# Kernel optimization log

Measured on AMD Instinct MI355X. Metric: run time of the kernel, lower is better.

The kernel has to match this reference:

```python
import jax, jax.numpy as jnp
import numpy as np

N_NODES = 100000
N_EDGES = 1600000
D_IN = 128
D_OUT = 128
EPS = 1e-5


def setup_inputs() -> dict:
    key = jax.random.key(0)
    k1, k2, k3, k4, k5 = jax.random.split(key, 5)
    x = jax.random.normal(k1, (N_NODES, D_IN), dtype=jnp.float32)
    row = jax.random.randint(k2, (N_EDGES,), 0, N_NODES, dtype=jnp.int64)
    col = jax.random.randint(k3, (N_EDGES,), 0, N_NODES, dtype=jnp.int64)
    adj_vals = jax.random.uniform(k4, (N_EDGES,), dtype=jnp.float32)
    # Xavier-uniform init for weight, zeros for bias (as in the torch module)
    limit = float(np.sqrt(6.0 / (D_IN + D_OUT)))
    weight = jax.random.uniform(k5, (D_IN, D_OUT), minval=-limit, maxval=limit, dtype=jnp.float32)
    bias = jnp.zeros((D_OUT,), dtype=jnp.float32)
    return {"x": x, "row": row, "col": col, "adj_vals": adj_vals, "weight": weight, "bias": bias}


def reference(x, row, col, adj_vals, weight, bias):
    # degree = row-sum of sparse adj
    degree = jax.ops.segment_sum(adj_vals, row, num_segments=N_NODES)
    degree = jnp.where(degree == 0, EPS, degree)
    d_inv_sqrt = (degree + EPS) ** -0.5  # [N]
    # edge-wise symmetric normalization: D^-1/2 A D^-1/2
    edge_w = d_inv_sqrt[row] * adj_vals * d_inv_sqrt[col]  # [E]
    # SpMM: gather neighbor features, scale, scatter-add to destination rows
    msgs = edge_w[:, None] * x[col]  # [E, D_IN]
    agg = jax.ops.segment_sum(msgs, row, num_segments=N_NODES)  # [N, D_IN]
    return agg @ weight + bias
```

## Files before the change

kernel.cpp:

```cpp
#include <hip/hip_runtime.h>

#define NN 100000
#define NE 1600000
#define D  128
#define EPS 1e-5f

#define NBKT   782
#define NEB    391
#define EPB_H  4096
#define NSCAN  (NBKT*NEB)
#define GRID2  299
#define CAP    2560

#define OFF_HCNT 0x0000000ULL
#define OFF_PART 0x0140000ULL
#define OFF_DINV 0x0150000ULL
#define OFF_GREC 0x0200000ULL
#define OFF_YB   0x0F00000ULL

typedef short short8 __attribute__((ext_vector_type(8)));
typedef float f32x4 __attribute__((ext_vector_type(4)));

static __device__ __forceinline__ unsigned f2bf(float f) {
    unsigned u = __float_as_uint(f);
    return (u + 0x7fffu + ((u >> 16) & 1u)) >> 16;
}

__global__ void k0h(const int* __restrict__ row, unsigned* __restrict__ hcnt) {
    __shared__ unsigned h[NBKT];
    int t = threadIdx.x, b = blockIdx.x;
    for (int i = t; i < NBKT; i += 256) h[i] = 0;
    __syncthreads();
    int ebeg = b * EPB_H;
    for (int i = t; i < EPB_H; i += 256) {
        int e = ebeg + i;
        if (e < NE) atomicAdd(&h[((unsigned)row[e]) >> 7], 1u);
    }
    __syncthreads();
    for (int i = t; i < NBKT; i += 256) hcnt[i * NEB + b] = h[i];
}

__global__ void k2a(const unsigned* __restrict__ hcnt, unsigned* __restrict__ part) {
    __shared__ unsigned s[256];
    int t = threadIdx.x;
    int gi = blockIdx.x * 1024 + t * 4;
    unsigned v = 0;
    #pragma unroll
    for (int j = 0; j < 4; ++j) if (gi + j < NSCAN) v += hcnt[gi + j];
    s[t] = v;
    __syncthreads();
    for (int d = 128; d > 0; d >>= 1) {
        if (t < d) s[t] += s[t + d];
        __syncthreads();
    }
    if (t == 0) part[blockIdx.x] = s[0];
}

__global__ void k2c(unsigned* __restrict__ hcnt, const unsigned* __restrict__ part) {
    __shared__ unsigned s[256];
    __shared__ unsigned bbase;
    int t = threadIdx.x, g = blockIdx.x;

    unsigned v = 0;
    for (int i = t; i < g; i += 256) v += part[i];
    s[t] = v;
    __syncthreads();
    for (int d = 128; d > 0; d >>= 1) {
        if (t < d) s[t] += s[t + d];
        __syncthreads();
    }
    if (t == 0) bbase = s[0];
    __syncthreads();
    unsigned base = bbase;
    __syncthreads();

    int gi = g * 1024 + t * 4;
    unsigned w[4], tot = 0;
    #pragma unroll
    for (int j = 0; j < 4; ++j) {
        w[j] = (gi + j < NSCAN) ? hcnt[gi + j] : 0;
        tot += w[j];
    }
    s[t] = tot;
    __syncthreads();
    for (int d = 1; d < 256; d <<= 1) {
        unsigned u = (t >= d) ? s[t - d] : 0;
        __syncthreads();
        s[t] += u;
        __syncthreads();
    }
    unsigned run = base + s[t] - tot;
    #pragma unroll
    for (int j = 0; j < 4; ++j) {
        if (gi + j < NSCAN) { hcnt[gi + j] = run; run += w[j]; }
    }
}

__launch_bounds__(256)
__global__ void k3(const int* __restrict__ row, const int* __restrict__ col,
                   const float* __restrict__ adj, const unsigned* __restrict__ hcnt,
                   unsigned long long* __restrict__ grec) {
    __shared__ unsigned cur[NBKT];
    int t = threadIdx.x, b = blockIdx.x;
    for (int i = t; i < NBKT; i += 256) cur[i] = hcnt[i * NEB + b];
    __syncthreads();
    int ebeg = b * EPB_H;
    for (int i = t; i < EPB_H; i += 256) {
        int e = ebeg + i;
        if (e >= NE) continue;
        unsigned r = (unsigned)row[e];
        unsigned aq = (unsigned)rintf(adj[e] * 32767.0f);
        unsigned lo = (unsigned)col[e] | (aq << 17);
        unsigned dst = atomicAdd(&cur[r >> 7], 1u);
        grec[dst] = (unsigned long long)lo | ((unsigned long long)(r & 127u) << 32);
    }
}

__launch_bounds__(256, 2)
__global__ void k1g(const float* __restrict__ x, const float* __restrict__ w,
                    const unsigned* __restrict__ hcnt,
                    const unsigned long long* __restrict__ grec,
                    float* __restrict__ dinv_g, unsigned short* __restrict__ yb) {
    __shared__ unsigned short sx[128 * 128];
    __shared__ unsigned short sw[128 * 128];
    __shared__ unsigned sdeg[128];
    __shared__ float sdv[128];
    int tid = threadIdx.x;
    int b = blockIdx.x;
    int base = b * 128;

    if (tid < 128) sdeg[tid] = 0;
    __syncthreads();
    unsigned beg = hcnt[b * NEB];
    unsigned end = (b == NBKT - 1) ? NE : hcnt[(b + 1) * NEB];
    for (unsigned p = beg + tid; p < end; p += 256) {
        unsigned long long rec = grec[p];
        atomicAdd(&sdeg[(unsigned)(rec >> 32) & 127u], ((unsigned)rec >> 17) & 0x7FFFu);
    }
    __syncthreads();
    if (tid < 128) {
        float d = (float)sdeg[tid] * (1.0f / 32767.0f);
        d = (d == 0.0f) ? EPS : d;
        float dv = rsqrtf(d + EPS);
        sdv[tid] = dv;
        int r = base + tid;
        if (r < NN) dinv_g[r] = dv;
    }

    #pragma unroll
    for (int i = 0; i < 8; ++i) {
        int task = i * 256 + tid;
        int n = task & 127, ko = task >> 7;
        const float* wp = w + (size_t)(ko * 8) * D + n;
        uint4 pk;
        pk.x = f2bf(wp[0])     | (f2bf(wp[D])     << 16);
        pk.y = f2bf(wp[2 * D]) | (f2bf(wp[3 * D]) << 16);
        pk.z = f2bf(wp[4 * D]) | (f2bf(wp[5 * D]) << 16);
        pk.w = f2bf(wp[6 * D]) | (f2bf(wp[7 * D]) << 16);
        int idx = (n * 128 + ko * 8) ^ ((n & 7) << 3);
        *(uint4*)(&sw[idx]) = pk;
    }
    #pragma unroll
    for (int i = 0; i < 8; ++i) {
        int task = i * 256 + tid;
        int ko = task & 15, r = task >> 4;
        int gr = base + r;
        float4 f0 = make_float4(0.f, 0.f, 0.f, 0.f), f1 = f0;
        if (gr < NN) {
            const float* xp = x + (size_t)gr * D + ko * 8;
            f0 = *(const float4*)xp;
            f1 = *(const float4*)(xp + 4);
        }
        uint4 pk;
        pk.x = f2bf(f0.x) | (f2bf(f0.y) << 16);
        pk.y = f2bf(f0.z) | (f2bf(f0.w) << 16);
        pk.z = f2bf(f1.x) | (f2bf(f1.y) << 16);
        pk.w = f2bf(f1.z) | (f2bf(f1.w) << 16);
        int idx = (r * 128 + ko * 8) ^ ((r & 7) << 3);
        *(uint4*)(&sx[idx]) = pk;
    }
    __syncthreads();

    int wv = tid >> 6, l = tid & 63;
    int lr = l & 15, g = l >> 4;

    f32x4 acc[2][8];
    #pragma unroll
    for (int ti = 0; ti < 2; ++ti)
        #pragma unroll
        for (int tj = 0; tj < 8; ++tj)
            acc[ti][tj] = (f32x4){0.f, 0.f, 0.f, 0.f};

    #pragma unroll
    for (int kc = 0; kc < 4; ++kc) {
        int kb = kc * 32 + g * 8;
        short8 a[2], bb[8];
        #pragma unroll
        for (int ti = 0; ti < 2; ++ti) {
            int r0 = wv * 32 + ti * 16 + lr;
            a[ti] = *(const short8*)(&sx[(r0 * 128 + kb) ^ ((r0 & 7) << 3)]);
        }
        #pragma unroll
        for (int tj = 0; tj < 8; ++tj) {
            int n0 = tj * 16 + lr;
            bb[tj] = *(const short8*)(&sw[(n0 * 128 + kb) ^ ((n0 & 7) << 3)]);
        }
        #pragma unroll
        for (int ti = 0; ti < 2; ++ti)
            #pragma unroll
            for (int tj = 0; tj < 8; ++tj)
                acc[ti][tj] = __builtin_amdgcn_mfma_f32_16x16x32_bf16(
                    a[ti], bb[tj], acc[ti][tj], 0, 0, 0);
    }

    #pragma unroll
    for (int ti = 0; ti < 2; ++ti) {
        #pragma unroll
        for (int reg = 0; reg < 4; ++reg) {
            int lrow = wv * 32 + ti * 16 + g * 4 + reg;
            int gr = base + lrow;
            if (gr < NN) {
                float dv = sdv[lrow];
                #pragma unroll
                for (int tj = 0; tj < 8; ++tj)
                    yb[(size_t)gr * D + tj * 16 + lr] =
                        (unsigned short)f2bf(acc[ti][tj][reg] * dv);
            }
        }
    }
}

__launch_bounds__(256, 4)
__global__ void k4b(const unsigned* __restrict__ hcnt, const unsigned long long* __restrict__ grec,
                    const float* __restrict__ dinv, const unsigned short* __restrict__ yb,
                    const float* __restrict__ bias, float* __restrict__ out) {
    __shared__ unsigned ecol[CAP + 16];
    __shared__ unsigned cnt[128], rb[128], cur[128], sc[128];
    int t = threadIdx.x, b = blockIdx.x;

    if (t < 128) cnt[t] = 0;
    __syncthreads();
    unsigned beg = hcnt[b * NEB];
    unsigned end = (b == NBKT - 1) ? NE : hcnt[(b + 1) * NEB];
    for (unsigned p = beg + t; p < end; p += 256)
        atomicAdd(&cnt[(unsigned)(grec[p] >> 32) & 127u], 1u);
    __syncthreads();

    if (t < 128) sc[t] = cnt[t];
    __syncthreads();
    for (int d = 1; d < 128; d <<= 1) {
        unsigned u = (t >= d && t < 128) ? sc[t - d] : 0;
        __syncthreads();
        if (t < 128) sc[t] += u;
        __syncthreads();
    }
    if (t < 128) { rb[t] = sc[t] - cnt[t]; cur[t] = sc[t] - cnt[t]; }
    __syncthreads();

    for (unsigned p = beg + t; p < end; p += 256) {
        unsigned long long rec = grec[p];
        unsigned rank = atomicAdd(&cur[(unsigned)(rec >> 32) & 127u], 1u);
        if (rank < CAP) ecol[rank] = (unsigned)rec;
    }
    __syncthreads();

    int grp = t >> 4, lq = t & 15;
    for (int k = 0; k < 8; ++k) {
        int rowlo = grp * 8 + k;
        int r = b * 128 + rowlo;
        if (r >= NN) continue;
        unsigned jb = rb[rowlo];
        unsigned c  = cnt[rowlo];
        unsigned jend = min(jb + c, (unsigned)CAP);

        float a0 = 0.f, a1 = 0.f, a2 = 0.f, a3 = 0.f;
        float a4 = 0.f, a5 = 0.f, a6 = 0.f, a7 = 0.f;

        for (unsigned j = jb; j < jend; j += 16) {
            unsigned ee[16];
            uint4 yq[16];
            float wv[16];
            int cm[16];
            #pragma unroll
            for (int u = 0; u < 16; ++u) ee[u] = ecol[j + u];
            #pragma unroll
            for (int u = 0; u < 16; ++u) cm[u] = min((int)(ee[u] & 0x1FFFFu), NN - 1);
            #pragma unroll
            for (int u = 0; u < 16; ++u)
                yq[u] = ((const uint4*)(yb + (size_t)cm[u] * D))[lq];
            #pragma unroll
            for (int u = 0; u < 16; ++u)
                wv[u] = (j + u < jend) ? (float)(ee[u] >> 17) : 0.f;
            #pragma unroll
            for (int u = 0; u < 16; ++u) {
                a0 += wv[u] * __uint_as_float(yq[u].x << 16);
                a1 += wv[u] * __uint_as_float(yq[u].x & 0xffff0000u);
                a2 += wv[u] * __uint_as_float(yq[u].y << 16);
                a3 += wv[u] * __uint_as_float(yq[u].y & 0xffff0000u);
                a4 += wv[u] * __uint_as_float(yq[u].z << 16);
                a5 += wv[u] * __uint_as_float(yq[u].z & 0xffff0000u);
                a6 += wv[u] * __uint_as_float(yq[u].w << 16);
                a7 += wv[u] * __uint_as_float(yq[u].w & 0xffff0000u);
            }
        }

        float scale = dinv[r] * (1.0f / 32767.0f);
        const float4* bp = (const float4*)bias + lq * 2;
        float4* op = (float4*)(out + (size_t)r * D) + lq * 2;
        float4 b0 = bp[0], b1 = bp[1];
        op[0] = make_float4(a0 * scale + b0.x, a1 * scale + b0.y,
                            a2 * scale + b0.z, a3 * scale + b0.w);
        op[1] = make_float4(a4 * scale + b1.x, a5 * scale + b1.y,
                            a6 * scale + b1.z, a7 * scale + b1.w);
    }
}

extern "C" void kernel_launch(void* const* d_in, const int* in_sizes, int n_in,
                              void* d_out, int out_size, void* d_ws, size_t ws_size,
                              hipStream_t stream) {
    const float* x    = (const float*)d_in[0];
    const int*   row  = (const int*)d_in[1];
    const int*   col  = (const int*)d_in[2];
    const float* adj  = (const float*)d_in[3];
    const float* wgt  = (const float*)d_in[4];
    const float* bias = (const float*)d_in[5];
    float* out = (float*)d_out;
    char*  ws  = (char*)d_ws;

    unsigned* hcnt  = (unsigned*)(ws + OFF_HCNT);
    unsigned* part  = (unsigned*)(ws + OFF_PART);
    float*    dinv  = (float*)(ws + OFF_DINV);
    unsigned long long* grec = (unsigned long long*)(ws + OFF_GREC);
    unsigned short* yb = (unsigned short*)(ws + OFF_YB);

    k0h<<<NEB, 256, 0, stream>>>(row, hcnt);
    k2a<<<GRID2, 256, 0, stream>>>(hcnt, part);
    k2c<<<GRID2, 256, 0, stream>>>(hcnt, part);
    k3 <<<NEB, 256, 0, stream>>>(row, col, adj, hcnt, grec);
    k1g<<<NBKT, 256, 0, stream>>>(x, wgt, hcnt, grec, dinv, yb);
    k4b<<<NBKT, 256, 0, stream>>>(hcnt, grec, dinv, yb, bias, out);
}
```

Measured before the change: 147.5 us.

## Move per-row edge sorting into k1g and split k4b columns across XCD-paired blocks

```diff
diff --git a/kernel.cpp b/kernel.cpp
--- a/kernel.cpp
+++ b/kernel.cpp
@@ -15,8 +15,10 @@
 #define OFF_HCNT 0x0000000ULL
 #define OFF_PART 0x0140000ULL
 #define OFF_DINV 0x0150000ULL
-#define OFF_GREC 0x0200000ULL
-#define OFF_YB   0x0F00000ULL
+#define OFF_RBC  0x0200000ULL
+#define OFF_GREC 0x0280000ULL
+#define OFF_ECOL 0x0F00000ULL
+#define OFF_YB   0x1700000ULL
 
 typedef short short8 __attribute__((ext_vector_type(8)));
 typedef float f32x4 __attribute__((ext_vector_type(4)));
@@ -120,24 +122,30 @@
 __global__ void k1g(const float* __restrict__ x, const float* __restrict__ w,
                     const unsigned* __restrict__ hcnt,
                     const unsigned long long* __restrict__ grec,
-                    float* __restrict__ dinv_g, unsigned short* __restrict__ yb) {
+                    float* __restrict__ dinv_g, unsigned* __restrict__ rbcnt_g,
+                    unsigned* __restrict__ ecol_g, unsigned short* __restrict__ yb) {
     __shared__ unsigned short sx[128 * 128];
     __shared__ unsigned short sw[128 * 128];
-    __shared__ unsigned sdeg[128];
+    __shared__ unsigned sdeg[128], scnt[128], srb[128], scur[128];
     __shared__ float sdv[128];
+    unsigned* secol = (unsigned*)sx;
     int tid = threadIdx.x;
     int b = blockIdx.x;
     int base = b * 128;
 
-    if (tid < 128) sdeg[tid] = 0;
+    if (tid < 128) { sdeg[tid] = 0; scnt[tid] = 0; }
     __syncthreads();
     unsigned beg = hcnt[b * NEB];
     unsigned end = (b == NBKT - 1) ? NE : hcnt[(b + 1) * NEB];
+    unsigned n = end - beg;
     for (unsigned p = beg + tid; p < end; p += 256) {
         unsigned long long rec = grec[p];
-        atomicAdd(&sdeg[(unsigned)(rec >> 32) & 127u], ((unsigned)rec >> 17) & 0x7FFFu);
-    }
-    __syncthreads();
+        unsigned rid = (unsigned)(rec >> 32) & 127u;
+        atomicAdd(&sdeg[rid], ((unsigned)rec >> 17) & 0x7FFFu);
+        atomicAdd(&scnt[rid], 1u);
+    }
+    __syncthreads();
+
     if (tid < 128) {
         float d = (float)sdeg[tid] * (1.0f / 32767.0f);
         d = (d == 0.0f) ? EPS : d;
@@ -145,19 +153,44 @@
         sdv[tid] = dv;
         int r = base + tid;
         if (r < NN) dinv_g[r] = dv;
-    }
+        srb[tid] = scnt[tid];
+    }
+    __syncthreads();
+    for (int dd = 1; dd < 128; dd <<= 1) {
+        unsigned u = (tid >= dd && tid < 128) ? srb[tid - dd] : 0;
+        __syncthreads();
+        if (tid < 128) srb[tid] += u;
+        __syncthreads();
+    }
+    if (tid < 128) {
+        unsigned rb = srb[tid] - scnt[tid];
+        srb[tid] = rb;
+        scur[tid] = rb;
+        rbcnt_g[b * 128 + tid] = (rb << 16) | scnt[tid];
+    }
+    __syncthreads();
+
+    for (unsigned p = beg + tid; p < end; p += 256) {
+        unsigned long long rec = grec[p];
+        unsigned rank = atomicAdd(&scur[(unsigned)(rec >> 32) & 127u], 1u);
+        if (rank < CAP) secol[rank] = (unsigned)rec;
+    }
+    __syncthreads();
+    unsigned ns = min(n, (unsigned)CAP);
+    for (unsigned i = tid; i < ns; i += 256) ecol_g[(size_t)b * CAP + i] = secol[i];
+    __syncthreads();
 
     #pragma unroll
     for (int i = 0; i < 8; ++i) {
         int task = i * 256 + tid;
-        int n = task & 127, ko = task >> 7;
-        const float* wp = w + (size_t)(ko * 8) * D + n;
+        int nn = task & 127, ko = task >> 7;
+        const float* wp = w + (size_t)(ko * 8) * D + nn;
         uint4 pk;
         pk.x = f2bf(wp[0])     | (f2bf(wp[D])     << 16);
         pk.y = f2bf(wp[2 * D]) | (f2bf(wp[3 * D]) << 16);
         pk.z = f2bf(wp[4 * D]) | (f2bf(wp[5 * D]) << 16);
         pk.w = f2bf(wp[6 * D]) | (f2bf(wp[7 * D]) << 16);
-        int idx = (n * 128 + ko * 8) ^ ((n & 7) << 3);
+        int idx = (nn * 128 + ko * 8) ^ ((nn & 7) << 3);
         *(uint4*)(&sw[idx]) = pk;
     }
     #pragma unroll
@@ -230,55 +263,45 @@
     }
 }
 
-__launch_bounds__(256, 4)
-__global__ void k4b(const unsigned* __restrict__ hcnt, const unsigned long long* __restrict__ grec,
+__launch_bounds__(512, 4)
+__global__ void k4b(const unsigned* __restrict__ rbcnt_g, const unsigned* __restrict__ ecol_g,
                     const float* __restrict__ dinv, const unsigned short* __restrict__ yb,
                     const float* __restrict__ bias, float* __restrict__ out) {
     __shared__ unsigned ecol[CAP + 16];
-    __shared__ unsigned cnt[128], rb[128], cur[128], sc[128];
-    int t = threadIdx.x, b = blockIdx.x;
-
-    if (t < 128) cnt[t] = 0;
-    __syncthreads();
-    unsigned beg = hcnt[b * NEB];
-    unsigned end = (b == NBKT - 1) ? NE : hcnt[(b + 1) * NEB];
-    for (unsigned p = beg + t; p < end; p += 256)
-        atomicAdd(&cnt[(unsigned)(grec[p] >> 32) & 127u], 1u);
-    __syncthreads();
-
-    if (t < 128) sc[t] = cnt[t];
-    __syncthreads();
-    for (int d = 1; d < 128; d <<= 1) {
-        unsigned u = (t >= d && t < 128) ? sc[t - d] : 0;
-        __syncthreads();
-        if (t < 128) sc[t] += u;
-        __syncthreads();
-    }
-    if (t < 128) { rb[t] = sc[t] - cnt[t]; cur[t] = sc[t] - cnt[t]; }
-    __syncthreads();
-
-    for (unsigned p = beg + t; p < end; p += 256) {
-        unsigned long long rec = grec[p];
-        unsigned rank = atomicAdd(&cur[(unsigned)(rec >> 32) & 127u], 1u);
-        if (rank < CAP) ecol[rank] = (unsigned)rec;
-    }
+    __shared__ unsigned rb_l[128], cnt_l[128];
+    __shared__ unsigned nsh;
+    int t = threadIdx.x, bid = blockIdx.x;
+    int xcd = bid & 7;
+    int ch  = xcd >> 2;
+    int q   = (bid >> 3) * 4 + (xcd & 3);
+    if (q >= NBKT) return;
+    int cb = ch * 64;
+
+    if (t < 128) {
+        unsigned v = rbcnt_g[q * 128 + t];
+        rb_l[t] = v >> 16;
+        cnt_l[t] = v & 0xFFFFu;
+        if (t == 127) nsh = min((v >> 16) + (v & 0xFFFFu), (unsigned)CAP);
+    }
+    __syncthreads();
+    unsigned n = nsh;
+    const unsigned* eg = ecol_g + (size_t)q * CAP;
+    for (unsigned i = t; i < n; i += 512) ecol[i] = eg[i];
     __syncthreads();
 
     int grp = t >> 4, lq = t & 15;
-    for (int k = 0; k < 8; ++k) {
-        int rowlo = grp * 8 + k;
-        int r = b * 128 + rowlo;
+    for (int k = 0; k < 4; ++k) {
+        int rowlo = grp * 4 + k;
+        int r = q * 128 + rowlo;
         if (r >= NN) continue;
-        unsigned jb = rb[rowlo];
-        unsigned c  = cnt[rowlo];
-        unsigned jend = min(jb + c, (unsigned)CAP);
+        unsigned jb = rb_l[rowlo];
+        unsigned jend = min(jb + cnt_l[rowlo], (unsigned)CAP);
 
         float a0 = 0.f, a1 = 0.f, a2 = 0.f, a3 = 0.f;
-        float a4 = 0.f, a5 = 0.f, a6 = 0.f, a7 = 0.f;
 
         for (unsigned j = jb; j < jend; j += 16) {
             unsigned ee[16];
-            uint4 yq[16];
+            uint2 yq[16];
             float wv[16];
             int cm[16];
             #pragma unroll
@@ -287,7 +310,7 @@
             for (int u = 0; u < 16; ++u) cm[u] = min((int)(ee[u] & 0x1FFFFu), NN - 1);
             #pragma unroll
             for (int u = 0; u < 16; ++u)
-                yq[u] = ((const uint4*)(yb + (size_t)cm[u] * D))[lq];
+                yq[u] = *(const uint2*)(yb + (size_t)cm[u] * D + cb + lq * 4);
             #pragma unroll
             for (int u = 0; u < 16; ++u)
                 wv[u] = (j + u < jend) ? (float)(ee[u] >> 17) : 0.f;
@@ -297,21 +320,14 @@
                 a1 += wv[u] * __uint_as_float(yq[u].x & 0xffff0000u);
                 a2 += wv[u] * __uint_as_float(yq[u].y << 16);
                 a3 += wv[u] * __uint_as_float(yq[u].y & 0xffff0000u);
-                a4 += wv[u] * __uint_as_float(yq[u].z << 16);
-                a5 += wv[u] * __uint_as_float(yq[u].z & 0xffff0000u);
-                a6 += wv[u] * __uint_as_float(yq[u].w << 16);
-                a7 += wv[u] * __uint_as_float(yq[u].w & 0xffff0000u);
             }
         }
 
         float scale = dinv[r] * (1.0f / 32767.0f);
-        const float4* bp = (const float4*)bias + lq * 2;
-        float4* op = (float4*)(out + (size_t)r * D) + lq * 2;
-        float4 b0 = bp[0], b1 = bp[1];
-        op[0] = make_float4(a0 * scale + b0.x, a1 * scale + b0.y,
-                            a2 * scale + b0.z, a3 * scale + b0.w);
-        op[1] = make_float4(a4 * scale + b1.x, a5 * scale + b1.y,
-                            a6 * scale + b1.z, a7 * scale + b1.w);
+        float4 bb = ((const float4*)(bias + cb))[lq];
+        float4 rr = make_float4(a0 * scale + bb.x, a1 * scale + bb.y,
+                                a2 * scale + bb.z, a3 * scale + bb.w);
+        ((float4*)(out + (size_t)r * D + cb))[lq] = rr;
     }
 }
 
@@ -330,13 +346,15 @@
     unsigned* hcnt  = (unsigned*)(ws + OFF_HCNT);
     unsigned* part  = (unsigned*)(ws + OFF_PART);
     float*    dinv  = (float*)(ws + OFF_DINV);
+    unsigned* rbcnt = (unsigned*)(ws + OFF_RBC);
     unsigned long long* grec = (unsigned long long*)(ws + OFF_GREC);
+    unsigned* ecolg = (unsigned*)(ws + OFF_ECOL);
     unsigned short* yb = (unsigned short*)(ws + OFF_YB);
 
     k0h<<<NEB, 256, 0, stream>>>(row, hcnt);
     k2a<<<GRID2, 256, 0, stream>>>(hcnt, part);
     k2c<<<GRID2, 256, 0, stream>>>(hcnt, part);
     k3 <<<NEB, 256, 0, stream>>>(row, col, adj, hcnt, grec);
-    k1g<<<NBKT, 256, 0, stream>>>(x, wgt, hcnt, grec, dinv, yb);
-    k4b<<<NBKT, 256, 0, stream>>>(hcnt, grec, dinv, yb, bias, out);
-}
+    k1g<<<NBKT, 256, 0, stream>>>(x, wgt, hcnt, grec, dinv, rbcnt, ecolg, yb);
+    k4b<<<1568, 512, 0, stream>>>(rbcnt, ecolg, dinv, yb, bias, out);
+}
```

New measurement: 137.9 us. -6.5%, faster.
